# Optimization experiments

Measured on AMD Instinct MI355X. Metric: run time of the kernel, lower is better.

Reference implementation:

```python
import jax, jax.numpy as jnp
import numpy as np

K = 4
H = 256
N0 = 65536
SIZES = [(65536, 32768), (32768, 8192), (8192, 2048)]  # (m_l, num_segments_l)


def setup_inputs() -> dict:
    key = jax.random.key(0)
    ks = jax.random.split(key, 20)
    inp = {}
    inp["x"] = jax.random.normal(ks[0], (N0, H), jnp.float32)
    inp["initial_map"] = jax.random.randint(ks[1], (N0,), 0, N0)
    prev = N0
    for l, (m, g) in enumerate(SIZES):
        # -1 is the 'no child' sentinel (maps to the prepended zero row after +1)
        inp[f"order_matrix_{l}"] = jax.random.randint(ks[2 + l], (K, m), -1, prev)
        inp[f"pooling_{l}"] = jnp.repeat(jnp.arange(g), m // g)  # covers all segments
        inp[f"type_mask_{l}"] = jax.random.randint(ks[6 + l], (m,), 0, 4)  # 0 leaf, 1 P, 2 Z, 3 S
        prev = g
    scale = 1.0 / np.sqrt(H).astype(np.float32)
    inp["W_z"] = jax.random.normal(ks[10], (K, H, H), jnp.float32) * scale
    inp["W_z_int"] = jax.random.normal(ks[11], (H, H), jnp.float32) * scale
    inp["W_s"] = jax.random.normal(ks[12], (K, H, H), jnp.float32) * scale
    inp["W_s_int"] = jax.random.normal(ks[13], (H, H), jnp.float32) * scale
    inp["W_p"] = jax.random.normal(ks[14], (H, H), jnp.float32) * scale
    inp["W_pf"] = jax.random.normal(ks[15], (H, H), jnp.float32) * scale
    return inp


def _layer(data, om, pool, tmask, g, W_z, W_z_int, W_s, W_s_int, W_p, W_pf):
    omp = om + 1                      # [K, m]; -1 -> 0 (zero row)
    empty = omp == 0                  # children that don't exist
    padded = jnp.concatenate([jnp.zeros((1, data.shape[1]), data.dtype), data], axis=0)
    gathered = padded[omp]            # [K, m, H]

    def type_sum(W):                  # per-child Linear, mask missing children, sum over children
        stack = jnp.einsum('kmh,koh->kmo', gathered, W)
        return jnp.where(empty[:, :, None], 0.0, stack).sum(axis=0)

    z_out = type_sum(W_z) @ W_z_int.T         # [m, H]
    s_out = type_sum(W_s) @ W_s_int.T         # [m, H]
    p_out = gathered[0] @ W_p.T               # [m, H]

    temp = gathered[0]                        # default: pass through first child (leaf type 0)
    temp = jnp.where((tmask == 2)[:, None], z_out, temp)
    temp = jnp.where((tmask == 3)[:, None], s_out, temp)
    temp = jnp.where((tmask == 1)[:, None], p_out, temp)
    temp = jnp.where(empty.all(axis=0)[:, None], 0.0, temp)

    pooled = jax.ops.segment_sum(temp, pool, num_segments=g)       # global_add_pool
    tm2 = jax.ops.segment_max(tmask, pool, num_segments=g)         # global_max_pool
    pooled = jnp.where((tm2 != 0)[:, None], jax.nn.elu(pooled), pooled)
    pooled = jnp.where((tm2 == 1)[:, None], pooled @ W_pf.T, pooled)
    return pooled


def reference(x, initial_map,
              order_matrix_0, pooling_0, type_mask_0,
              order_matrix_1, pooling_1, type_mask_1,
              order_matrix_2, pooling_2, type_mask_2,
              W_z, W_z_int, W_s, W_s_int, W_p, W_pf):
    oms = [order_matrix_0, order_matrix_1, order_matrix_2]
    pools = [pooling_0, pooling_1, pooling_2]
    tmasks = [type_mask_0, type_mask_1, type_mask_2]
    data = x[initial_map]
    for l, (m, g) in enumerate(SIZES):
        data = _layer(data, oms[l], pools[l], tmasks[l], g,
                      W_z, W_z_int, W_s, W_s_int, W_p, W_pf)
    return data
```

## Files before the change

kernel.cpp:

```cpp
#include <hip/hip_runtime.h>
#include <math.h>

#define H 256

typedef __attribute__((ext_vector_type(8))) short bf16x8;
typedef __attribute__((ext_vector_type(4))) float f32x4;
typedef __attribute__((ext_vector_type(4))) short short4v;

__device__ __forceinline__ short f2bf(float f) {
  union { float f; unsigned u; } x;
  x.f = f;
  unsigned r = x.u + 0x7fffu + ((x.u >> 16) & 1u);
  return (short)(r >> 16);
}
__device__ __forceinline__ float bf2f(short s) {
  union { float f; unsigned u; } x;
  x.u = ((unsigned)(unsigned short)s) << 16;
  return x.f;
}

__global__ __launch_bounds__(256) void gather_cvt_kernel(const float4* __restrict__ x,
                                                         const int* __restrict__ map,
                                                         short4v* __restrict__ out, int n) {
  int total = n * (H / 4);
  for (int idx = blockIdx.x * blockDim.x + threadIdx.x; idx < total;
       idx += gridDim.x * blockDim.x) {
    int e = idx >> 6;
    int q = idx & 63;
    float4 v = x[(size_t)map[e] * 64 + q];
    short4v s;
    s[0] = f2bf(v.x); s[1] = f2bf(v.y); s[2] = f2bf(v.z); s[3] = f2bf(v.w);
    out[idx] = s;
  }
}

__global__ __launch_bounds__(256) void wprep_kernel(
    const float* __restrict__ Wz, const float* __restrict__ Wzint,
    const float* __restrict__ Ws, const float* __restrict__ Wsint,
    const float* __restrict__ Wp, const float* __restrict__ Wpf,
    short* __restrict__ Wbf, int* __restrict__ zero_base) {
  int bid = blockIdx.x;
  int tid = threadIdx.x;
  if (bid < 2048) {
    const float* Wint = (bid < 1024) ? Wzint : Wsint;
    const float* W1 = (bid < 1024) ? Wz : Ws;
    short* out = Wbf + ((bid < 1024) ? 131072 : 393216);
    int b = bid & 1023;
    int k = b >> 8, o = b & 255;
    const float* A = Wint + (size_t)o * 256;
    const float* B = W1 + (size_t)k * 65536;
    float acc = 0.f;
#pragma unroll 8
    for (int j = 0; j < 256; ++j) acc = fmaf(A[j], B[(size_t)j * 256 + tid], acc);
    out[((size_t)k * 256 + o) * 256 + tid] = f2bf(acc);
  } else if (bid < 2176) {
    int i4 = (bid - 2048) * 256 + tid;
    int e = i4 * 4;
    const float* src = (e < 65536) ? Wp : Wpf;
    int off = (e < 65536) ? e : e - 65536;
    float4 v = *(const float4*)(src + off);
    short4v o;
    o[0] = f2bf(v.x); o[1] = f2bf(v.y); o[2] = f2bf(v.z); o[3] = f2bf(v.w);
    *(short4v*)(Wbf + e) = o;
  } else {
    if (tid < 192) zero_base[tid] = 0;
  }
}

__device__ __forceinline__ void bucket_body(const int* __restrict__ tmask, int base,
                                            int m, int g, int r,
                                            int* __restrict__ lists,
                                            int* __restrict__ counts,
                                            int* __restrict__ tm2,
                                            int* __restrict__ listF,
                                            int* __restrict__ cntF) {
  __shared__ int lc[4];
  __shared__ int lbase[4];
  int tid = threadIdx.x;
  if (tid < 4) lc[tid] = 0;
  __syncthreads();
  int i = base * 256 + tid;
  int t = 0, rank = 0;
  bool ok = i < m;
  if (ok) {
    t = tmask[i];
    rank = atomicAdd(&lc[t], 1);
  }
  __syncthreads();
  if (tid < 4) lbase[tid] = atomicAdd(&counts[tid], lc[tid]);
  __syncthreads();
  if (ok) lists[t * m + lbase[t] + rank] = i;

  int s = i;
  if (s < g) {
    int t2 = 0;
    for (int j = 0; j < r; ++j) {
      int tt = tmask[s * r + j];
      t2 = tt > t2 ? tt : t2;
    }
    tm2[s] = t2;
    unsigned long long mask = __ballot(t2 == 1);
    if (t2 == 1) {
      int lane = tid & 63;
      unsigned long long lt = (lane == 0) ? 0ull : (~0ull >> (64 - lane));
      int rnk = __popcll(mask & lt);
      int leader = __ffsll((long long)mask) - 1;
      int b = 0;
      if (lane == leader) b = atomicAdd(cntF, __popcll(mask));
      b = __shfl(b, leader);
      listF[b + rnk] = s;
    }
  }
}

__global__ __launch_bounds__(256) void bucket_all_kernel(
    const int* __restrict__ tm0, const int* __restrict__ tm1, const int* __restrict__ tm2in,
    int* __restrict__ lists0, int* __restrict__ lists1, int* __restrict__ lists2,
    int* __restrict__ counts,
    int* __restrict__ seg0, int* __restrict__ seg1, int* __restrict__ seg2,
    int* __restrict__ listF0, int* __restrict__ listF1, int* __restrict__ listF2) {
  int bid = blockIdx.x;
  if (bid < 256)
    bucket_body(tm0, bid, 65536, 32768, 2, lists0, counts, seg0, listF0, counts + 4);
  else if (bid < 384)
    bucket_body(tm1, bid - 256, 32768, 8192, 4, lists1, counts + 8, seg1, listF1, counts + 12);
  else
    bucket_body(tm2in, bid - 384, 8192, 2048, 4, lists2, counts + 16, seg2, listF2, counts + 20);
}

template <int NCH>
__device__ __forceinline__ void gemm_tile(const short* __restrict__ Abf,
                                          const int* __restrict__ om, int m,
                                          const int* __restrict__ list, int n,
                                          int rowbase, int cg,
                                          const short* __restrict__ W1,
                                          const short* __restrict__ zrow,
                                          short* __restrict__ temp, char* lds) {
  const int tid = threadIdx.x;
  const int lane = tid & 63;
  const int wave = tid >> 6;
  const int lr = lane & 15;
  const int kg = lane >> 4;
  const int wrow = rowbase + wave * 32;

  int cidx[2][NCH];
#pragma unroll
  for (int rt = 0; rt < 2; ++rt) {
    int i = wrow + rt * 16 + lr;
    int rid = (i < n) ? list[i] : -1;
#pragma unroll
    for (int k = 0; k < NCH; ++k) cidx[rt][k] = (rid >= 0) ? om[k * m + rid] : -1;
  }

  f32x4 acc[2][4];
#pragma unroll
  for (int rt = 0; rt < 2; ++rt)
#pragma unroll
    for (int c = 0; c < 4; ++c) {
      f32x4 z = {0.f, 0.f, 0.f, 0.f};
      acc[rt][c] = z;
    }

  for (int kc = 0; kc < NCH; ++kc) {
    const short* ap[2];
#pragma unroll
    for (int rt = 0; rt < 2; ++rt) {
      int c = cidx[rt][kc];
      ap[rt] = (c >= 0) ? (Abf + (size_t)c * 256 + kg * 8) : (zrow + kg * 8);
    }

    const char* psrc = (const char*)W1 + ((size_t)kc * 256 + cg * 64) * 512;
    __syncthreads();
#pragma unroll
    for (int it = 0; it < 8; ++it) {
      int idx = it * 4096 + tid * 16;
      bf16x8 v = *(const bf16x8*)(psrc + idx);
      int col = idx >> 9;
      *(bf16x8*)(lds + (idx ^ ((col & 7) << 4))) = v;
    }
    __syncthreads();

#pragma unroll
    for (int ko = 0; ko < 8; ++ko) {
      bf16x8 a[2], b[4];
#pragma unroll
      for (int c = 0; c < 4; ++c) {
        int col = c * 16 + lr;
        int off = (col * 512 + ko * 64 + kg * 16) ^ ((col & 7) << 4);
        b[c] = *(const bf16x8*)(lds + off);
      }
#pragma unroll
      for (int rt = 0; rt < 2; ++rt) a[rt] = *(const bf16x8*)(ap[rt] + ko * 32);
#pragma unroll
      for (int rt = 0; rt < 2; ++rt)
#pragma unroll
        for (int c = 0; c < 4; ++c)
          acc[rt][c] =
              __builtin_amdgcn_mfma_f32_16x16x32_bf16(a[rt], b[c], acc[rt][c], 0, 0, 0);
    }
  }

#pragma unroll
  for (int rt = 0; rt < 2; ++rt) {
#pragma unroll
    for (int q = 0; q < 4; ++q) {
      int i2 = wrow + rt * 16 + kg * 4 + q;
      if (i2 >= n) continue;
      int row = list[i2];
      short* dst = temp + (size_t)row * 256 + cg * 64 + lr;
#pragma unroll
      for (int c = 0; c < 4; ++c) dst[c * 16] = f2bf(acc[rt][c][q]);
    }
  }
}

__global__ __launch_bounds__(256) void fused_gemm(
    const short* __restrict__ Abf, const int* __restrict__ om, int m,
    const int* __restrict__ lists, const int* __restrict__ counts,
    const short* __restrict__ Wp,
    const short* __restrict__ Wcz, const short* __restrict__ Wcs,
    const short* __restrict__ zrow,
    short* __restrict__ temp) {
  const int c14 = (m >> 7) << 2;
  int bid = (int)blockIdx.x;
  __shared__ __align__(16) char lds[64 * 512];

  int type, item;
  if (bid < c14)            { type = 2; item = bid; }
  else if (bid < 2 * c14)   { type = 3; item = bid - c14; }
  else if (bid < 3 * c14)   { type = 1; item = bid - 2 * c14; }
  else                      { type = 0; item = bid - 3 * c14; }

  int n = counts[type];
  const int* list = lists + type * m;

  if (type == 0) {
    int rowbase = item * 64;
    if (rowbase >= n) return;
    int lim = n - rowbase;
    if (lim > 64) lim = 64;
    for (int idx = threadIdx.x; idx < lim * 32; idx += 256) {
      int e = rowbase + (idx >> 5);
      int q = idx & 31;
      int row = list[e];
      int c = om[row];
      bf16x8 v = {0, 0, 0, 0, 0, 0, 0, 0};
      if (c >= 0) v = *(const bf16x8*)(Abf + (size_t)c * 256 + q * 8);
      *(bf16x8*)(temp + (size_t)row * 256 + q * 8) = v;
    }
    return;
  }

  int rowtile = ((item >> 5) << 3) | (item & 7);
  int cg = (item >> 3) & 3;
  int rowbase = rowtile * 128;
  if (rowbase >= n) return;

  if (type == 1)
    gemm_tile<1>(Abf, om, m, list, n, rowbase, cg, Wp, zrow, temp, lds);
  else if (type == 2)
    gemm_tile<4>(Abf, om, m, list, n, rowbase, cg, Wcz, zrow, temp, lds);
  else
    gemm_tile<4>(Abf, om, m, list, n, rowbase, cg, Wcs, zrow, temp, lds);
}

__global__ __launch_bounds__(256) void reduce_kernel(const short* __restrict__ temp,
                                                     int r, int g,
                                                     const int* __restrict__ tm2,
                                                     float* __restrict__ outf,
                                                     short* __restrict__ outbf) {
  int idx = blockIdx.x * 256 + threadIdx.x;
  if (idx >= g * 32) return;
  int s = idx >> 5;
  int q = idx & 31;
  float acc[8];
#pragma unroll
  for (int k = 0; k < 8; ++k) acc[k] = 0.f;
  for (int j = 0; j < r; ++j) {
    bf16x8 v = *(const bf16x8*)(temp + (size_t)(s * r + j) * 256 + q * 8);
#pragma unroll
    for (int k = 0; k < 8; ++k) acc[k] += bf2f(v[k]);
  }
  if (tm2[s] != 0) {
#pragma unroll
    for (int k = 0; k < 8; ++k) acc[k] = acc[k] > 0.f ? acc[k] : (expf(acc[k]) - 1.f);
  }
  if (outf) {
    float4 f0 = {acc[0], acc[1], acc[2], acc[3]};
    float4 f1 = {acc[4], acc[5], acc[6], acc[7]};
    *(float4*)(outf + (size_t)s * 256 + q * 8) = f0;
    *(float4*)(outf + (size_t)s * 256 + q * 8 + 4) = f1;
  }
  if (outbf) {
    bf16x8 o;
#pragma unroll
    for (int k = 0; k < 8; ++k) o[k] = f2bf(acc[k]);
    *(bf16x8*)(outbf + (size_t)s * 256 + q * 8) = o;
  }
}

template <int SRC>
__global__ __launch_bounds__(256) void pf_gemm(short* __restrict__ buf,
                                               float* __restrict__ fbuf,
                                               const int* __restrict__ listF,
                                               const int* __restrict__ cnt,
                                               const short* __restrict__ Wpf) {
  int n = *cnt;
  int rowbase = blockIdx.x * 32;
  if (rowbase >= n) return;
  const int lane = threadIdx.x & 63;
  const int wave = threadIdx.x >> 6;
  const int colbase = wave * 64;
  const int lr = lane & 15;
  const int kg = lane >> 4;

  int src[2];
#pragma unroll
  for (int rt = 0; rt < 2; ++rt) {
    int i = rowbase + rt * 16 + lr;
    src[rt] = (i < n) ? listF[i] : -1;
  }

  f32x4 acc[2][4];
#pragma unroll
  for (int rt = 0; rt < 2; ++rt)
#pragma unroll
    for (int c = 0; c < 4; ++c) {
      f32x4 z = {0.f, 0.f, 0.f, 0.f};
      acc[rt][c] = z;
    }

#pragma unroll 2
  for (int ko = 0; ko < 256; ko += 32) {
    bf16x8 b[4];
#pragma unroll
    for (int c = 0; c < 4; ++c)
      b[c] = *(const bf16x8*)(Wpf + (size_t)(colbase + c * 16 + lr) * 256 + ko + kg * 8);
#pragma unroll
    for (int rt = 0; rt < 2; ++rt) {
      bf16x8 a = {0, 0, 0, 0, 0, 0, 0, 0};
      if (src[rt] >= 0) {
        if (SRC == 0) {
          a = *(const bf16x8*)(buf + (size_t)src[rt] * 256 + ko + kg * 8);
        } else {
          const float* p = fbuf + (size_t)src[rt] * 256 + ko + kg * 8;
          float4 u0 = *(const float4*)p;
          float4 u1 = *(const float4*)(p + 4);
          a[0] = f2bf(u0.x); a[1] = f2bf(u0.y); a[2] = f2bf(u0.z); a[3] = f2bf(u0.w);
          a[4] = f2bf(u1.x); a[5] = f2bf(u1.y); a[6] = f2bf(u1.z); a[7] = f2bf(u1.w);
        }
      }
#pragma unroll
      for (int c = 0; c < 4; ++c)
        acc[rt][c] = __builtin_amdgcn_mfma_f32_16x16x32_bf16(a, b[c], acc[rt][c], 0, 0, 0);
    }
  }

  __syncthreads();

#pragma unroll
  for (int rt = 0; rt < 2; ++rt) {
#pragma unroll
    for (int q = 0; q < 4; ++q) {
      int i2 = rowbase + rt * 16 + kg * 4 + q;
      if (i2 >= n) continue;
      int c2 = listF[i2];
      if (SRC == 0) {
        short* db = buf + (size_t)c2 * 256 + colbase + lr;
#pragma unroll
        for (int c = 0; c < 4; ++c) db[c * 16] = f2bf(acc[rt][c][q]);
      } else {
        float* df = fbuf + (size_t)c2 * 256 + colbase + lr;
#pragma unroll
        for (int c = 0; c < 4; ++c) df[c * 16] = acc[rt][c][q];
      }
    }
  }
}

extern "C" void kernel_launch(void* const* d_in, const int* in_sizes, int n_in,
                              void* d_out, int out_size, void* d_ws, size_t ws_size,
                              hipStream_t stream) {
  const float* x = (const float*)d_in[0];
  const int* initial_map = (const int*)d_in[1];
  const int* om[3] = {(const int*)d_in[2], (const int*)d_in[5], (const int*)d_in[8]};
  const int* tmask[3] = {(const int*)d_in[4], (const int*)d_in[7], (const int*)d_in[10]};
  const float* W_z = (const float*)d_in[11];
  const float* W_z_int = (const float*)d_in[12];
  const float* W_s = (const float*)d_in[13];
  const float* W_s_int = (const float*)d_in[14];
  const float* W_p = (const float*)d_in[15];
  const float* W_pf = (const float*)d_in[16];

  char* base = (char*)d_ws;
  short* d0bf  = (short*)(base);
  short* temp0 = (short*)(base + 33554432);
  short* d1bf  = (short*)(base);
  short* temp1 = (short*)(base + 16777216);
  short* d2bf  = (short*)(base + 33554432);
  short* temp2 = (short*)(base + 37748736);
  size_t off = 67108864;
  short* Wbf = (short*)(base + off); off += 655360 * 2;
  int* lists0 = (int*)(base + off); off += 4u * 65536 * 4;
  int* lists1 = (int*)(base + off); off += 4u * 32768 * 4;
  int* lists2 = (int*)(base + off); off += 4u * 8192 * 4;
  int* listF0 = (int*)(base + off); off += 32768 * 4;
  int* listF1 = (int*)(base + off); off += 8192 * 4;
  int* listF2 = (int*)(base + off); off += 2048 * 4;
  int* seg0 = (int*)(base + off); off += 32768 * 4;
  int* seg1 = (int*)(base + off); off += 8192 * 4;
  int* seg2 = (int*)(base + off); off += 2048 * 4;
  int* counts = (int*)(base + off); off += 256;
  short* zrow = (short*)(base + off); off += 512;

  short* Wp_bf  = Wbf + 0;
  short* Wpf_bf = Wbf + 65536;
  short* Wcz_bf = Wbf + 131072;
  short* Wcs_bf = Wbf + 393216;

  hipLaunchKernelGGL(wprep_kernel, dim3(2177), dim3(256), 0, stream, W_z, W_z_int,
                     W_s, W_s_int, W_p, W_pf, Wbf, counts);
  hipLaunchKernelGGL(bucket_all_kernel, dim3(416), dim3(256), 0, stream,
                     tmask[0], tmask[1], tmask[2], lists0, lists1, lists2, counts,
                     seg0, seg1, seg2, listF0, listF1, listF2);
  hipLaunchKernelGGL(gather_cvt_kernel, dim3(2048), dim3(256), 0, stream,
                     (const float4*)x, initial_map, (short4v*)d0bf, 65536);

  const int Ms[3] = {65536, 32768, 8192};
  const int Gs[3] = {32768, 8192, 2048};
  const short* dinbf[3] = {d0bf, d1bf, d2bf};
  short* tempL[3] = {temp0, temp1, temp2};
  short* nextbf[3] = {d1bf, d2bf, nullptr};
  int* listsL[3] = {lists0, lists1, lists2};
  int* listFL[3] = {listF0, listF1, listF2};
  int* segL[3] = {seg0, seg1, seg2};

  for (int l = 0; l < 3; ++l) {
    int m = Ms[l], g = Gs[l], r = m / g;
    int c14 = (m >> 7) << 2;
    int grid = 3 * c14 + m / 64;
    hipLaunchKernelGGL(fused_gemm, dim3(grid), dim3(256), 0, stream, dinbf[l], om[l],
                       m, listsL[l], counts + l * 8, Wp_bf, Wcz_bf, Wcs_bf, zrow,
                       tempL[l]);

    hipLaunchKernelGGL(reduce_kernel, dim3(g * 32 / 256), dim3(256), 0, stream,
                       tempL[l], r, g, segL[l], (l == 2) ? (float*)d_out : nullptr,
                       nextbf[l]);

    if (l < 2)
      hipLaunchKernelGGL((pf_gemm<0>), dim3(g / 32), dim3(256), 0, stream, nextbf[l],
                         (float*)nullptr, listFL[l], counts + l * 8 + 4, Wpf_bf);
    else
      hipLaunchKernelGGL((pf_gemm<1>), dim3(g / 32), dim3(256), 0, stream,
                         (short*)nullptr, (float*)d_out, listFL[l], counts + l * 8 + 4,
                         Wpf_bf);
  }
}
```

Measured before the change: 217.7 us.

## Double-buffer weight tiles in LDS with register prefetch of next chunk

```diff
diff --git a/kernel.cpp b/kernel.cpp
--- a/kernel.cpp
+++ b/kernel.cpp
@@ -161,7 +161,32 @@
       acc[rt][c] = z;
     }
 
+  {
+    const char* p0 = (const char*)W1 + ((size_t)cg * 64) * 512;
+    bf16x8 breg[8];
+#pragma unroll
+    for (int it = 0; it < 8; ++it)
+      breg[it] = *(const bf16x8*)(p0 + it * 4096 + tid * 16);
+#pragma unroll
+    for (int it = 0; it < 8; ++it) {
+      int idx = it * 4096 + tid * 16;
+      int col = idx >> 9;
+      *(bf16x8*)(lds + (idx ^ ((col & 7) << 4))) = breg[it];
+    }
+  }
+  __syncthreads();
+
   for (int kc = 0; kc < NCH; ++kc) {
+    char* curbuf = lds + (kc & 1) * 32768;
+
+    bf16x8 breg[8];
+    if (kc + 1 < NCH) {
+      const char* pn = (const char*)W1 + ((size_t)(kc + 1) * 256 + cg * 64) * 512;
+#pragma unroll
+      for (int it = 0; it < 8; ++it)
+        breg[it] = *(const bf16x8*)(pn + it * 4096 + tid * 16);
+    }
+
     const short* ap[2];
 #pragma unroll
     for (int rt = 0; rt < 2; ++rt) {
@@ -169,17 +194,6 @@
       ap[rt] = (c >= 0) ? (Abf + (size_t)c * 256 + kg * 8) : (zrow + kg * 8);
     }
 
-    const char* psrc = (const char*)W1 + ((size_t)kc * 256 + cg * 64) * 512;
-    __syncthreads();
-#pragma unroll
-    for (int it = 0; it < 8; ++it) {
-      int idx = it * 4096 + tid * 16;
-      bf16x8 v = *(const bf16x8*)(psrc + idx);
-      int col = idx >> 9;
-      *(bf16x8*)(lds + (idx ^ ((col & 7) << 4))) = v;
-    }
-    __syncthreads();
-
 #pragma unroll
     for (int ko = 0; ko < 8; ++ko) {
       bf16x8 a[2], b[4];
@@ -187,7 +201,7 @@
       for (int c = 0; c < 4; ++c) {
         int col = c * 16 + lr;
         int off = (col * 512 + ko * 64 + kg * 16) ^ ((col & 7) << 4);
-        b[c] = *(const bf16x8*)(lds + off);
+        b[c] = *(const bf16x8*)(curbuf + off);
       }
 #pragma unroll
       for (int rt = 0; rt < 2; ++rt) a[rt] = *(const bf16x8*)(ap[rt] + ko * 32);
@@ -197,6 +211,17 @@
         for (int c = 0; c < 4; ++c)
           acc[rt][c] =
               __builtin_amdgcn_mfma_f32_16x16x32_bf16(a[rt], b[c], acc[rt][c], 0, 0, 0);
+    }
+
+    if (kc + 1 < NCH) {
+      char* nb = lds + ((kc + 1) & 1) * 32768;
+#pragma unroll
+      for (int it = 0; it < 8; ++it) {
+        int idx = it * 4096 + tid * 16;
+        int col = idx >> 9;
+        *(bf16x8*)(nb + (idx ^ ((col & 7) << 4))) = breg[it];
+      }
+      __syncthreads();
     }
   }
 
@@ -223,7 +248,7 @@
     short* __restrict__ temp) {
   const int c14 = (m >> 7) << 2;
   int bid = (int)blockIdx.x;
-  __shared__ __align__(16) char lds[64 * 512];
+  __shared__ __align__(16) char lds[2 * 32768];
 
   int type, item;
   if (bid < c14)            { type = 2; item = bid; }
```

After: 229.9 us. 5.6% more time.
